# Performance work log

Measured on AMD Instinct MI355X. Metric: run time of the kernel, lower is better.

The kernel has to match this reference:

```python
import jax, jax.numpy as jnp
import numpy as np

ATT = 256
NUM_GENES = 2128
HIDDEN = 512
B, T = 128, 1024


def setup_inputs() -> dict:
    key = jax.random.key(0)
    ks = jax.random.split(key, 8)
    return {
        "genes": jax.random.normal(ks[0], (B, NUM_GENES), dtype=jnp.float32),
        "smiles": jax.random.normal(ks[1], (B, T, HIDDEN), dtype=jnp.float32),
        "w_num_gene_features": jax.random.normal(ks[2], (1,), dtype=jnp.float32) * 0.1,
        "w_genes": jax.random.normal(ks[3], (NUM_GENES, ATT), dtype=jnp.float32) * 0.1,
        "b_genes": jax.random.normal(ks[4], (ATT,), dtype=jnp.float32) * 0.1,
        "dense_kernel": jax.random.normal(ks[5], (HIDDEN, ATT), dtype=jnp.float32) * 0.05,
        "dense_bias": jnp.zeros((ATT,), dtype=jnp.float32),
        "v": jax.random.normal(ks[6], (ATT,), dtype=jnp.float32) * 0.1,
    }


def reference(genes, smiles, w_num_gene_features, w_genes, b_genes,
              dense_kernel, dense_bias, v):
    # genes: [B, G]; collapse trivial feature axis via scalar weight -> [B, G]
    genes_collapsed = genes * w_num_gene_features[0]
    # gene context: [B, A]
    gene_proj = genes_collapsed @ w_genes + b_genes
    # smiles projection: [B, T, A]
    smiles_proj = jnp.einsum('bth,ha->bta', smiles, dense_kernel) + dense_bias
    # additive attention energies
    x = jnp.tanh(gene_proj[:, None, :] + smiles_proj)          # [B, T, A]
    xv = jnp.einsum('bta,a->bt', x, v)                          # [B, T]
    alphas = jax.nn.softmax(xv, axis=-1)                        # [B, T]
    output = jnp.einsum('bth,bt->bh', smiles, alphas)           # [B, H]
    return output, alphas
```

## Files before the change

kernel.cpp:

```cpp
#include <hip/hip_runtime.h>
#include <stdint.h>

#define B_ 128
#define T_ 1024
#define H_ 512
#define A_ 256
#define G_ 2128

typedef short s16x8 __attribute__((ext_vector_type(8)));
typedef float f32x4 __attribute__((ext_vector_type(4)));
typedef unsigned int u32;

__device__ inline unsigned short f2bf(float f) {
  unsigned u = __float_as_uint(f);
  u += 0x7fff + ((u >> 16) & 1);
  return (unsigned short)(u >> 16);
}
__device__ inline unsigned pack2bf(float a, float b) {
  return ((unsigned)f2bf(b) << 16) | f2bf(a);
}
__device__ inline float bf_lo(unsigned u) { return __uint_as_float(u << 16); }
__device__ inline float bf_hi(unsigned u) { return __uint_as_float(u & 0xffff0000u); }
__device__ inline float fast_tanh(float x) {
  x = fminf(15.f, fmaxf(-15.f, x));
  float e = __expf(2.f * x);
  return (e - 1.f) * __builtin_amdgcn_rcpf(e + 1.f);
}
__device__ inline void gl_lds16(const void* g, void* l) {
  __builtin_amdgcn_global_load_lds(
      (const __attribute__((address_space(1))) u32*)g,
      (__attribute__((address_space(3))) u32*)l, 16, 0, 0);
}

__global__ void prep_kt(const float* __restrict__ K,
                        unsigned short* __restrict__ khi) {
  int idx = blockIdx.x * 256 + threadIdx.x;
  int h = idx >> 8;
  int a = idx & 255;
  int kb = h >> 5, k = h & 31;
  int grp = k >> 3, sub = k & 7;
  khi[kb * 8192 + a * 32 + ((grp ^ (a & 3)) * 8) + sub] = f2bf(K[idx]);
}

__global__ __launch_bounds__(256) void gene_proj_k(
    const float* __restrict__ genes, const float* __restrict__ w0p,
    const float* __restrict__ Wg, const float* __restrict__ bg,
    const float* __restrict__ db, float* __restrict__ gp4) {
  __shared__ float sg[532];
  int b = blockIdx.x;
  int gc = blockIdx.y;
  int a = threadIdx.x;
  int g0 = gc * 532;
  for (int i = threadIdx.x; i < 532; i += 256) sg[i] = genes[(size_t)b * G_ + g0 + i];
  __syncthreads();
  float s = 0.f;
  #pragma unroll 8
  for (int g = 0; g < 532; ++g)
    s = fmaf(sg[g], Wg[(size_t)(g0 + g) * A_ + a], s);
  float val = w0p[0] * s;
  if (gc == 0) val += bg[a] + db[a];
  gp4[(gc * B_ + b) * A_ + a] = val;
}

__global__ __launch_bounds__(256, 2) void pass1(
    const float* __restrict__ smiles, const unsigned short* __restrict__ khi,
    unsigned short* __restrict__ smb, const float* __restrict__ gp4,
    const float* __restrict__ v, float* __restrict__ xv) {
  __shared__ unsigned short sA[128 * 32];
  __shared__ unsigned short sB[256 * 32];
  __shared__ float sXV[128 * 4];

  const int tid = threadIdx.x;
  const int b = blockIdx.y;
  const int tb = blockIdx.x;
  const int lane = tid & 63;
  const int w = tid >> 6;
  const int n = lane & 15;
  const int q = lane >> 4;

  const int ar = tid >> 1;
  const int half = tid & 1;
  const int g0 = half * 2;
  const int s0 = (g0 ^ (ar & 3)) * 8;
  const int s1 = ((g0 + 1) ^ (ar & 3)) * 8;
  const float* asrc = smiles + ((size_t)(b * 1024 + tb * 128 + ar)) * 512 + half * 16;
  unsigned short* adst = smb + (((size_t)(b * 8 + tb)) * 16) * 4096 + ar * 32;

  f32x4 acc[8][4];
  #pragma unroll
  for (int i = 0; i < 8; ++i)
    #pragma unroll
    for (int j = 0; j < 4; ++j)
      acc[i][j] = (f32x4){0.f, 0.f, 0.f, 0.f};

  float4 f0 = *reinterpret_cast<const float4*>(asrc);
  float4 f1 = *reinterpret_cast<const float4*>(asrc + 4);
  float4 f2 = *reinterpret_cast<const float4*>(asrc + 8);
  float4 f3 = *reinterpret_cast<const float4*>(asrc + 12);

  for (int kb = 0; kb < 16; ++kb) {
    __builtin_amdgcn_sched_barrier(0);
    __builtin_amdgcn_s_barrier();
    __builtin_amdgcn_sched_barrier(0);

    uint4 p0, p1;
    p0.x = pack2bf(f0.x, f0.y); p0.y = pack2bf(f0.z, f0.w);
    p0.z = pack2bf(f1.x, f1.y); p0.w = pack2bf(f1.z, f1.w);
    p1.x = pack2bf(f2.x, f2.y); p1.y = pack2bf(f2.z, f2.w);
    p1.z = pack2bf(f3.x, f3.y); p1.w = pack2bf(f3.z, f3.w);
    *reinterpret_cast<uint4*>(&sA[ar * 32 + s0]) = p0;
    *reinterpret_cast<uint4*>(&sA[ar * 32 + s1]) = p1;
    __builtin_amdgcn_sched_barrier(0);
    #pragma unroll
    for (int r = 0; r < 4; ++r)
      gl_lds16(khi + kb * 8192 + w * 2048 + r * 512 + lane * 8,
               &sB[w * 2048 + r * 512]);
    __builtin_amdgcn_sched_barrier(0);
    {
      int noff = (kb < 15) ? (kb + 1) * 32 : 0;
      f0 = *reinterpret_cast<const float4*>(asrc + noff);
      f1 = *reinterpret_cast<const float4*>(asrc + noff + 4);
      f2 = *reinterpret_cast<const float4*>(asrc + noff + 8);
      f3 = *reinterpret_cast<const float4*>(asrc + noff + 12);
    }
    *reinterpret_cast<uint4*>(adst + kb * 4096 + s0) = p0;
    *reinterpret_cast<uint4*>(adst + kb * 4096 + s1) = p1;
    asm volatile("s_waitcnt vmcnt(6) lgkmcnt(0)" ::: "memory");
    __builtin_amdgcn_sched_barrier(0);
    __builtin_amdgcn_s_barrier();
    __builtin_amdgcn_sched_barrier(0);

    s16x8 af[8], bh[4];
    const int sw = (q ^ (n & 3)) * 8;
    #pragma unroll
    for (int j = 0; j < 4; ++j)
      bh[j] = *reinterpret_cast<const s16x8*>(&sB[(w * 64 + j * 16 + n) * 32 + sw]);
    #pragma unroll
    for (int i = 0; i < 8; ++i)
      af[i] = *reinterpret_cast<const s16x8*>(&sA[(i * 16 + n) * 32 + sw]);
    #pragma unroll
    for (int i = 0; i < 8; ++i)
      #pragma unroll
      for (int j = 0; j < 4; ++j)
        acc[i][j] = __builtin_amdgcn_mfma_f32_16x16x32_bf16(af[i], bh[j], acc[i][j], 0, 0, 0);
  }

  float vv[4], gg[4];
  #pragma unroll
  for (int j = 0; j < 4; ++j) {
    int a = w * 64 + j * 16 + n;
    int idx = b * A_ + a;
    vv[j] = v[a];
    gg[j] = gp4[idx] + gp4[B_ * A_ + idx] + gp4[2 * B_ * A_ + idx] +
            gp4[3 * B_ * A_ + idx];
  }
  #pragma unroll
  for (int i = 0; i < 8; ++i) {
    #pragma unroll
    for (int r = 0; r < 4; ++r) {
      float s = 0.f;
      #pragma unroll
      for (int j = 0; j < 4; ++j)
        s += vv[j] * fast_tanh(acc[i][j][r] + gg[j]);
      s += __shfl_xor(s, 1); s += __shfl_xor(s, 2);
      s += __shfl_xor(s, 4); s += __shfl_xor(s, 8);
      if (n == 0) sXV[(i * 16 + q * 4 + r) * 4 + w] = s;
    }
  }
  __syncthreads();
  if (tid < 128) {
    float* p = &sXV[tid * 4];
    xv[(size_t)b * T_ + tb * 128 + tid] = p[0] + p[1] + p[2] + p[3];
  }
}

__global__ __launch_bounds__(256) void softmax_k(const float* __restrict__ xv,
                                                 float* __restrict__ alphas) {
  __shared__ float red[8];
  int b = blockIdx.x, tid = threadIdx.x;
  float4 x = *reinterpret_cast<const float4*>(xv + b * T_ + tid * 4);
  float m = fmaxf(fmaxf(x.x, x.y), fmaxf(x.z, x.w));
  #pragma unroll
  for (int o = 1; o < 64; o <<= 1) m = fmaxf(m, __shfl_xor(m, o));
  if ((tid & 63) == 0) red[tid >> 6] = m;
  __syncthreads();
  m = fmaxf(fmaxf(red[0], red[1]), fmaxf(red[2], red[3]));
  float e0 = __expf(x.x - m), e1 = __expf(x.y - m);
  float e2 = __expf(x.z - m), e3 = __expf(x.w - m);
  float s = e0 + e1 + e2 + e3;
  #pragma unroll
  for (int o = 1; o < 64; o <<= 1) s += __shfl_xor(s, o);
  if ((tid & 63) == 0) red[4 + (tid >> 6)] = s;
  __syncthreads();
  s = red[4] + red[5] + red[6] + red[7];
  float inv = 1.f / s;
  float4 o4;
  o4.x = e0 * inv; o4.y = e1 * inv; o4.z = e2 * inv; o4.w = e3 * inv;
  *reinterpret_cast<float4*>(alphas + b * T_ + tid * 4) = o4;
}

__global__ __launch_bounds__(256) void pass3(const unsigned short* __restrict__ smb,
                                             const float* __restrict__ alphas,
                                             float* __restrict__ out) {
  __shared__ float red[3][64][8];
  int b = blockIdx.y, ts = blockIdx.x;
  int tid = threadIdx.x;
  int hg = tid & 63, tq = tid >> 6;
  int kb = hg >> 2, g = hg & 3;
  float acc[8] = {0.f, 0.f, 0.f, 0.f, 0.f, 0.f, 0.f, 0.f};
  for (int tb = ts * 2; tb < ts * 2 + 2; ++tb) {
    const unsigned short* tile = smb + (((size_t)b * 8 + tb) * 16 + kb) * 4096;
    const float* al = alphas + b * T_ + tb * 128;
    #pragma unroll 4
    for (int tt = 0; tt < 32; ++tt) {
      int tp = tq * 32 + tt;
      float a = al[tp];
      uint4 d = *reinterpret_cast<const uint4*>(tile + tp * 32 + ((g ^ (tp & 3)) * 8));
      acc[0] = fmaf(a, bf_lo(d.x), acc[0]); acc[1] = fmaf(a, bf_hi(d.x), acc[1]);
      acc[2] = fmaf(a, bf_lo(d.y), acc[2]); acc[3] = fmaf(a, bf_hi(d.y), acc[3]);
      acc[4] = fmaf(a, bf_lo(d.z), acc[4]); acc[5] = fmaf(a, bf_hi(d.z), acc[5]);
      acc[6] = fmaf(a, bf_lo(d.w), acc[6]); acc[7] = fmaf(a, bf_hi(d.w), acc[7]);
    }
  }
  if (tq) {
    #pragma unroll
    for (int e = 0; e < 8; ++e) red[tq - 1][hg][e] = acc[e];
  }
  __syncthreads();
  if (tq == 0) {
    float* op = out + (size_t)b * H_ + kb * 32 + g * 8;
    #pragma unroll
    for (int e = 0; e < 8; ++e)
      atomicAdd(op + e, acc[e] + red[0][hg][e] + red[1][hg][e] + red[2][hg][e]);
  }
}

extern "C" void kernel_launch(void* const* d_in, const int* in_sizes, int n_in,
                              void* d_out, int out_size, void* d_ws, size_t ws_size,
                              hipStream_t stream) {
  const float* genes  = (const float*)d_in[0];
  const float* smiles = (const float*)d_in[1];
  const float* w0     = (const float*)d_in[2];
  const float* wg     = (const float*)d_in[3];
  const float* bg     = (const float*)d_in[4];
  const float* dk     = (const float*)d_in[5];
  const float* db     = (const float*)d_in[6];
  const float* v      = (const float*)d_in[7];
  float* out = (float*)d_out;
  char* ws = (char*)d_ws;
  float* gp4 = (float*)ws;
  unsigned short* khi = (unsigned short*)(ws + 524288);
  float* xv = (float*)(ws + 524288 + 262144);
  unsigned short* smb = (unsigned short*)(ws + (2 << 20));
  float* alphas = out + B_ * H_;

  hipMemsetAsync(out, 0, B_ * H_ * sizeof(float), stream);
  prep_kt<<<512, 256, 0, stream>>>(dk, khi);
  gene_proj_k<<<dim3(B_, 4), 256, 0, stream>>>(genes, w0, wg, bg, db, gp4);
  pass1<<<dim3(8, B_), 256, 0, stream>>>(smiles, khi, smb, gp4, v, xv);
  softmax_k<<<B_, 256, 0, stream>>>(xv, alphas);
  pass3<<<dim3(4, B_), 256, 0, stream>>>(smb, alphas, out);
}
```

Before: 499.5 us.

## Fuse softmax and weighted sum into projection kernel with split-softmax merge

Replaces the separate softmax and weighted-sum passes with a per-tile local softmax inside the projection kernel, followed by an online-softmax merge kernel across the 8 tiles per batch. The tile's fp32 smiles rows are re-read right after the MFMA stage, so the bf16 staging copy and its readback are no longer needed. This also drops the output memset and the atomics. In exchange, the re-read of each tile depends on cache hits and adds a serial reduction loop to the end of the kernel.

```diff
diff --git a/kernel.cpp b/kernel.cpp
--- a/kernel.cpp
+++ b/kernel.cpp
@@ -19,8 +19,6 @@
 __device__ inline unsigned pack2bf(float a, float b) {
   return ((unsigned)f2bf(b) << 16) | f2bf(a);
 }
-__device__ inline float bf_lo(unsigned u) { return __uint_as_float(u << 16); }
-__device__ inline float bf_hi(unsigned u) { return __uint_as_float(u & 0xffff0000u); }
 __device__ inline float fast_tanh(float x) {
   x = fminf(15.f, fmaxf(-15.f, x));
   float e = __expf(2.f * x);
@@ -62,13 +60,15 @@
   gp4[(gc * B_ + b) * A_ + a] = val;
 }
 
-__global__ __launch_bounds__(256, 2) void pass1(
+__global__ __launch_bounds__(256, 2) void fused1(
     const float* __restrict__ smiles, const unsigned short* __restrict__ khi,
-    unsigned short* __restrict__ smb, const float* __restrict__ gp4,
-    const float* __restrict__ v, float* __restrict__ xv) {
+    const float* __restrict__ gp4, const float* __restrict__ v,
+    float* __restrict__ xv, float* __restrict__ ml, float* __restrict__ outp) {
   __shared__ unsigned short sA[128 * 32];
   __shared__ unsigned short sB[256 * 32];
   __shared__ float sXV[128 * 4];
+  __shared__ float sP[128];
+  __shared__ float sRed[8];
 
   const int tid = threadIdx.x;
   const int b = blockIdx.y;
@@ -84,7 +84,6 @@
   const int s0 = (g0 ^ (ar & 3)) * 8;
   const int s1 = ((g0 + 1) ^ (ar & 3)) * 8;
   const float* asrc = smiles + ((size_t)(b * 1024 + tb * 128 + ar)) * 512 + half * 16;
-  unsigned short* adst = smb + (((size_t)(b * 8 + tb)) * 16) * 4096 + ar * 32;
 
   f32x4 acc[8][4];
   #pragma unroll
@@ -123,9 +122,7 @@
       f2 = *reinterpret_cast<const float4*>(asrc + noff + 8);
       f3 = *reinterpret_cast<const float4*>(asrc + noff + 12);
     }
-    *reinterpret_cast<uint4*>(adst + kb * 4096 + s0) = p0;
-    *reinterpret_cast<uint4*>(adst + kb * 4096 + s1) = p1;
-    asm volatile("s_waitcnt vmcnt(6) lgkmcnt(0)" ::: "memory");
+    asm volatile("s_waitcnt vmcnt(4) lgkmcnt(0)" ::: "memory");
     __builtin_amdgcn_sched_barrier(0);
     __builtin_amdgcn_s_barrier();
     __builtin_amdgcn_sched_barrier(0);
@@ -168,71 +165,76 @@
     }
   }
   __syncthreads();
+
+  float xvv = -1e30f;
   if (tid < 128) {
     float* p = &sXV[tid * 4];
-    xv[(size_t)b * T_ + tb * 128 + tid] = p[0] + p[1] + p[2] + p[3];
-  }
-}
-
-__global__ __launch_bounds__(256) void softmax_k(const float* __restrict__ xv,
-                                                 float* __restrict__ alphas) {
-  __shared__ float red[8];
+    xvv = p[0] + p[1] + p[2] + p[3];
+    xv[(size_t)b * T_ + tb * 128 + tid] = xvv;
+  }
+  float mx = xvv;
+  #pragma unroll
+  for (int o = 1; o < 64; o <<= 1) mx = fmaxf(mx, __shfl_xor(mx, o));
+  if (lane == 0) sRed[w] = mx;
+  __syncthreads();
+  mx = fmaxf(fmaxf(sRed[0], sRed[1]), fmaxf(sRed[2], sRed[3]));
+  float e = (tid < 128) ? __expf(xvv - mx) : 0.f;
+  float lsum = e;
+  #pragma unroll
+  for (int o = 1; o < 64; o <<= 1) lsum += __shfl_xor(lsum, o);
+  if (lane == 0) sRed[4 + w] = lsum;
+  if (tid < 128) sP[tid] = e;
+  __syncthreads();
+  if (tid == 0) {
+    float l = sRed[4] + sRed[5] + sRed[6] + sRed[7];
+    ml[(b * 8 + tb) * 2] = mx;
+    ml[(b * 8 + tb) * 2 + 1] = l;
+  }
+
+  float2 a2 = {0.f, 0.f};
+  const float* sm2 = smiles + ((size_t)(b * 1024 + tb * 128)) * 512 + tid * 2;
+  #pragma unroll 8
+  for (int t = 0; t < 128; ++t) {
+    float a = sP[t];
+    float2 sv = *reinterpret_cast<const float2*>(sm2 + (size_t)t * 512);
+    a2.x = fmaf(a, sv.x, a2.x);
+    a2.y = fmaf(a, sv.y, a2.y);
+  }
+  *reinterpret_cast<float2*>(outp + ((size_t)(b * 8 + tb)) * 512 + tid * 2) = a2;
+}
+
+__global__ __launch_bounds__(256) void merge_k(
+    const float* __restrict__ ml, const float* __restrict__ outp,
+    const float* __restrict__ xv, float* __restrict__ out,
+    float* __restrict__ alphas) {
   int b = blockIdx.x, tid = threadIdx.x;
-  float4 x = *reinterpret_cast<const float4*>(xv + b * T_ + tid * 4);
-  float m = fmaxf(fmaxf(x.x, x.y), fmaxf(x.z, x.w));
-  #pragma unroll
-  for (int o = 1; o < 64; o <<= 1) m = fmaxf(m, __shfl_xor(m, o));
-  if ((tid & 63) == 0) red[tid >> 6] = m;
-  __syncthreads();
-  m = fmaxf(fmaxf(red[0], red[1]), fmaxf(red[2], red[3]));
-  float e0 = __expf(x.x - m), e1 = __expf(x.y - m);
-  float e2 = __expf(x.z - m), e3 = __expf(x.w - m);
-  float s = e0 + e1 + e2 + e3;
-  #pragma unroll
-  for (int o = 1; o < 64; o <<= 1) s += __shfl_xor(s, o);
-  if ((tid & 63) == 0) red[4 + (tid >> 6)] = s;
-  __syncthreads();
-  s = red[4] + red[5] + red[6] + red[7];
-  float inv = 1.f / s;
-  float4 o4;
-  o4.x = e0 * inv; o4.y = e1 * inv; o4.z = e2 * inv; o4.w = e3 * inv;
-  *reinterpret_cast<float4*>(alphas + b * T_ + tid * 4) = o4;
-}
-
-__global__ __launch_bounds__(256) void pass3(const unsigned short* __restrict__ smb,
-                                             const float* __restrict__ alphas,
-                                             float* __restrict__ out) {
-  __shared__ float red[3][64][8];
-  int b = blockIdx.y, ts = blockIdx.x;
-  int tid = threadIdx.x;
-  int hg = tid & 63, tq = tid >> 6;
-  int kb = hg >> 2, g = hg & 3;
-  float acc[8] = {0.f, 0.f, 0.f, 0.f, 0.f, 0.f, 0.f, 0.f};
-  for (int tb = ts * 2; tb < ts * 2 + 2; ++tb) {
-    const unsigned short* tile = smb + (((size_t)b * 8 + tb) * 16 + kb) * 4096;
-    const float* al = alphas + b * T_ + tb * 128;
-    #pragma unroll 4
-    for (int tt = 0; tt < 32; ++tt) {
-      int tp = tq * 32 + tt;
-      float a = al[tp];
-      uint4 d = *reinterpret_cast<const uint4*>(tile + tp * 32 + ((g ^ (tp & 3)) * 8));
-      acc[0] = fmaf(a, bf_lo(d.x), acc[0]); acc[1] = fmaf(a, bf_hi(d.x), acc[1]);
-      acc[2] = fmaf(a, bf_lo(d.y), acc[2]); acc[3] = fmaf(a, bf_hi(d.y), acc[3]);
-      acc[4] = fmaf(a, bf_lo(d.z), acc[4]); acc[5] = fmaf(a, bf_hi(d.z), acc[5]);
-      acc[6] = fmaf(a, bf_lo(d.w), acc[6]); acc[7] = fmaf(a, bf_hi(d.w), acc[7]);
-    }
-  }
-  if (tq) {
-    #pragma unroll
-    for (int e = 0; e < 8; ++e) red[tq - 1][hg][e] = acc[e];
-  }
-  __syncthreads();
-  if (tq == 0) {
-    float* op = out + (size_t)b * H_ + kb * 32 + g * 8;
-    #pragma unroll
-    for (int e = 0; e < 8; ++e)
-      atomicAdd(op + e, acc[e] + red[0][hg][e] + red[1][hg][e] + red[2][hg][e]);
-  }
+  float m[8], lq[8];
+  float M = -1e30f;
+  #pragma unroll
+  for (int q = 0; q < 8; ++q) {
+    m[q] = ml[(b * 8 + q) * 2];
+    lq[q] = ml[(b * 8 + q) * 2 + 1];
+    M = fmaxf(M, m[q]);
+  }
+  float L = 0.f, wq[8];
+  #pragma unroll
+  for (int q = 0; q < 8; ++q) {
+    wq[q] = __expf(m[q] - M);
+    L = fmaf(lq[q], wq[q], L);
+  }
+  float invL = 1.f / L;
+  float2 o2 = {0.f, 0.f};
+  #pragma unroll
+  for (int q = 0; q < 8; ++q) {
+    float2 p = *reinterpret_cast<const float2*>(outp + ((size_t)(b * 8 + q)) * 512 + tid * 2);
+    o2.x = fmaf(wq[q], p.x, o2.x);
+    o2.y = fmaf(wq[q], p.y, o2.y);
+  }
+  o2.x *= invL; o2.y *= invL;
+  *reinterpret_cast<float2*>(out + (size_t)b * H_ + tid * 2) = o2;
+  #pragma unroll
+  for (int t = tid; t < T_; t += 256)
+    alphas[(size_t)b * T_ + t] = __expf(xv[(size_t)b * T_ + t] - M) * invL;
 }
 
 extern "C" void kernel_launch(void* const* d_in, const int* in_sizes, int n_in,
@@ -250,14 +252,13 @@
   char* ws = (char*)d_ws;
   float* gp4 = (float*)ws;
   unsigned short* khi = (unsigned short*)(ws + 524288);
-  float* xv = (float*)(ws + 524288 + 262144);
-  unsigned short* smb = (unsigned short*)(ws + (2 << 20));
+  float* xv   = (float*)(ws + 786432);
+  float* ml   = (float*)(ws + 1310720);
+  float* outp = (float*)(ws + 1318912);
   float* alphas = out + B_ * H_;
 
-  hipMemsetAsync(out, 0, B_ * H_ * sizeof(float), stream);
   prep_kt<<<512, 256, 0, stream>>>(dk, khi);
   gene_proj_k<<<dim3(B_, 4), 256, 0, stream>>>(genes, w0, wg, bg, db, gp4);
-  pass1<<<dim3(8, B_), 256, 0, stream>>>(smiles, khi, smb, gp4, v, xv);
-  softmax_k<<<B_, 256, 0, stream>>>(xv, alphas);
-  pass3<<<dim3(4, B_), 256, 0, stream>>>(smb, alphas, out);
-}
+  fused1<<<dim3(8, B_), 256, 0, stream>>>(smiles, khi, gp4, v, xv, ml, outp);
+  merge_k<<<B_, 256, 0, stream>>>(ml, outp, xv, out, alphas);
+}
```

Result: faster. 485.9 us (-2.7%).
